# Kernel optimization log

Measured on AMD Instinct MI355X. Metric: run time of the kernel, lower is better.

Reference implementation:

```python
import jax, jax.numpy as jnp
import numpy as np

IN_DIM, HID, OUT, N_EXTRA, NTASKS, BATCH = 1024, 2048, 10, 3, 10, 4096
LOGSTD_MEAN, LOGSTD_STD = -6.0, 0.1


def setup_inputs() -> dict:
    key = jax.random.key(0)
    ks = jax.random.split(key, 20)
    n = lambda k, s: jax.random.normal(k, s, dtype=jnp.float32)
    return {
        "x": n(ks[0], (BATCH, IN_DIM)),
        # shared layer 0 (in_dim -> hidden)
        "mu_w0": n(ks[1], (HID, IN_DIM)) * (1.0 / np.sqrt(IN_DIM)),
        "ls_w0": LOGSTD_MEAN + LOGSTD_STD * n(ks[2], (HID, IN_DIM)),
        "mu_b0": n(ks[3], (HID,)) * 0.01,
        "ls_b0": LOGSTD_MEAN + LOGSTD_STD * n(ks[4], (HID,)),
        # shared layers 1..3 (hidden -> hidden), stacked
        "mu_w": n(ks[5], (N_EXTRA, HID, HID)) * (1.0 / np.sqrt(HID)),
        "ls_w": LOGSTD_MEAN + LOGSTD_STD * n(ks[6], (N_EXTRA, HID, HID)),
        "mu_b": n(ks[7], (N_EXTRA, HID)) * 0.01,
        "ls_b": LOGSTD_MEAN + LOGSTD_STD * n(ks[8], (N_EXTRA, HID)),
        # per-task heads (hidden -> out), stacked over tasks
        "mu_hw": n(ks[9], (NTASKS, OUT, HID)) * (1.0 / np.sqrt(HID)),
        "ls_hw": LOGSTD_MEAN + LOGSTD_STD * n(ks[10], (NTASKS, OUT, HID)),
        "mu_hb": n(ks[11], (NTASKS, OUT)) * 0.01,
        "ls_hb": LOGSTD_MEAN + LOGSTD_STD * n(ks[12], (NTASKS, OUT)),
        # reparameterization noise (one sample per forward, as in torch module)
        "eps_w0": n(ks[13], (HID, IN_DIM)),
        "eps_b0": n(ks[14], (HID,)),
        "eps_w": n(ks[15], (N_EXTRA, HID, HID)),
        "eps_b": n(ks[16], (N_EXTRA, HID)),
        "eps_hw": n(ks[17], (NTASKS, OUT, HID)),
        "eps_hb": n(ks[18], (NTASKS, OUT)),
        "task": jax.random.randint(ks[19], (BATCH,), 0, NTASKS, dtype=jnp.int64),
    }


def reference(x, mu_w0, ls_w0, mu_b0, ls_b0, mu_w, ls_w, mu_b, ls_b,
              mu_hw, ls_hw, mu_hb, ls_hb,
              eps_w0, eps_b0, eps_w, eps_b, eps_hw, eps_hb, task):
    # BayesianLinear: w = mu + exp(log_sigma) * eps
    w0 = mu_w0 + jnp.exp(ls_w0) * eps_w0          # [HID, IN]
    b0 = mu_b0 + jnp.exp(ls_b0) * eps_b0          # [HID]
    h = jax.nn.relu(x @ w0.T + b0)                # [B, HID]
    for i in range(N_EXTRA):                      # fixed small layer loop
        wi = mu_w[i] + jnp.exp(ls_w[i]) * eps_w[i]
        bi = mu_b[i] + jnp.exp(ls_b[i]) * eps_b[i]
        h = jax.nn.relu(h @ wi.T + bi)
    # multihead: compute every head, zero out non-matching rows (dense masked)
    hw = mu_hw + jnp.exp(ls_hw) * eps_hw          # [T, OUT, HID]
    hb = mu_hb + jnp.exp(ls_hb) * eps_hb          # [T, OUT]
    out_all = jnp.einsum('bh,toh->bto', h, hw) + hb[None]   # [B, T, OUT]
    onehot = (task[:, None] == jnp.arange(NTASKS)[None, :]).astype(h.dtype)
    return jnp.einsum('bto,bt->bo', out_all, onehot)        # [B, OUT]
```

## Files before the change

kernel.cpp:

```cpp
#include <hip/hip_runtime.h>
#include <cstdint>

#define BATCH 4096
#define IN_DIM 1024
#define HID 2048
#define OUT_DIM 10
#define NTASKS 10

typedef __bf16 bf16x8 __attribute__((ext_vector_type(8)));
typedef float f32x4 __attribute__((ext_vector_type(4)));
typedef __attribute__((address_space(3))) uint8_t lds_u8;
typedef const __attribute__((address_space(1))) uint8_t glb_u8;

__device__ __forceinline__ unsigned short f2bf(float f) {
    uint32_t u = __builtin_bit_cast(uint32_t, f);
    u += 0x7fffu + ((u >> 16) & 1u);
    return (unsigned short)(u >> 16);
}
__device__ __forceinline__ float bf2f(unsigned short h) {
    uint32_t u = ((uint32_t)h) << 16;
    return __builtin_bit_cast(float, u);
}


__global__ __launch_bounds__(256) void bl_transform(
    const float4* __restrict__ mu, const float4* __restrict__ ls,
    const float4* __restrict__ eps, ushort4* __restrict__ out)
{
    const int i0 = blockIdx.x * 1024 + threadIdx.x;
    const float4 m0 = mu[i0], m1 = mu[i0 + 256], m2 = mu[i0 + 512], m3 = mu[i0 + 768];
    const float4 l0 = ls[i0], l1 = ls[i0 + 256], l2 = ls[i0 + 512], l3 = ls[i0 + 768];
    const float4 e0 = eps[i0], e1 = eps[i0 + 256], e2 = eps[i0 + 512], e3 = eps[i0 + 768];
    ushort4 r0, r1, r2, r3;
    r0.x = f2bf(m0.x + __expf(l0.x) * e0.x); r0.y = f2bf(m0.y + __expf(l0.y) * e0.y);
    r0.z = f2bf(m0.z + __expf(l0.z) * e0.z); r0.w = f2bf(m0.w + __expf(l0.w) * e0.w);
    r1.x = f2bf(m1.x + __expf(l1.x) * e1.x); r1.y = f2bf(m1.y + __expf(l1.y) * e1.y);
    r1.z = f2bf(m1.z + __expf(l1.z) * e1.z); r1.w = f2bf(m1.w + __expf(l1.w) * e1.w);
    r2.x = f2bf(m2.x + __expf(l2.x) * e2.x); r2.y = f2bf(m2.y + __expf(l2.y) * e2.y);
    r2.z = f2bf(m2.z + __expf(l2.z) * e2.z); r2.w = f2bf(m2.w + __expf(l2.w) * e2.w);
    r3.x = f2bf(m3.x + __expf(l3.x) * e3.x); r3.y = f2bf(m3.y + __expf(l3.y) * e3.y);
    r3.z = f2bf(m3.z + __expf(l3.z) * e3.z); r3.w = f2bf(m3.w + __expf(l3.w) * e3.w);
    out[i0]       = r0;
    out[i0 + 256] = r1;
    out[i0 + 512] = r2;
    out[i0 + 768] = r3;
}

__global__ __launch_bounds__(256) void bl_cvt(
    const float4* __restrict__ in, ushort4* __restrict__ out)
{
    const int i0 = blockIdx.x * 1024 + threadIdx.x;
    const float4 v0 = in[i0], v1 = in[i0 + 256], v2 = in[i0 + 512], v3 = in[i0 + 768];
    ushort4 r0, r1, r2, r3;
    r0.x = f2bf(v0.x); r0.y = f2bf(v0.y); r0.z = f2bf(v0.z); r0.w = f2bf(v0.w);
    r1.x = f2bf(v1.x); r1.y = f2bf(v1.y); r1.z = f2bf(v1.z); r1.w = f2bf(v1.w);
    r2.x = f2bf(v2.x); r2.y = f2bf(v2.y); r2.z = f2bf(v2.z); r2.w = f2bf(v2.w);
    r3.x = f2bf(v3.x); r3.y = f2bf(v3.y); r3.z = f2bf(v3.z); r3.w = f2bf(v3.w);
    out[i0]       = r0;
    out[i0 + 256] = r1;
    out[i0 + 512] = r2;
    out[i0 + 768] = r3;
}

__global__ __launch_bounds__(256) void bl_small(
    const float* __restrict__ mu_b0, const float* __restrict__ ls_b0, const float* __restrict__ eps_b0,
    const float* __restrict__ mu_b,  const float* __restrict__ ls_b,  const float* __restrict__ eps_b,
    const float* __restrict__ mu_hw, const float* __restrict__ ls_hw, const float* __restrict__ eps_hw,
    const float* __restrict__ mu_hb, const float* __restrict__ ls_hb, const float* __restrict__ eps_hb,
    float* __restrict__ b_all, float* __restrict__ hw, float* __restrict__ hb)
{
    const int total = HID + 3*HID + NTASKS*OUT_DIM*HID + NTASKS*OUT_DIM;
    int i = blockIdx.x * blockDim.x + threadIdx.x;
    const int stride = gridDim.x * blockDim.x;
    for (; i < total; i += stride) {
        if (i < HID) {
            b_all[i] = mu_b0[i] + __expf(ls_b0[i]) * eps_b0[i];
        } else if (i < 4*HID) {
            const int j = i - HID;
            b_all[HID + j] = mu_b[j] + __expf(ls_b[j]) * eps_b[j];
        } else if (i < 4*HID + NTASKS*OUT_DIM*HID) {
            const int j = i - 4*HID;
            hw[j] = mu_hw[j] + __expf(ls_hw[j]) * eps_hw[j];
        } else {
            const int j = i - (4*HID + NTASKS*OUT_DIM*HID);
            hb[j] = mu_hb[j] + __expf(ls_hb[j]) * eps_hb[j];
        }
    }
}

#define BAR()        asm volatile("s_barrier" ::: "memory")
#define WAIT_LGKM0() do { asm volatile("s_waitcnt lgkmcnt(0)" ::: "memory"); __builtin_amdgcn_sched_barrier(0); } while (0)
#define RD_A(m, o)   (*(const bf16x8*)(ldsb + acur + (o) + (m)*2048))
#define RD_B(n, o)   (*(const bf16x8*)(ldsb + bcur + (o) + (n)*2048))
#define MFMA(d, va, vb) d = __builtin_amdgcn_mfma_f32_16x16x32_bf16(va, vb, d, 0, 0, 0)
#define STAGEI(i, kel, sl) \
    __builtin_amdgcn_global_load_lds((glb_u8*)(gsrc[i] + (kel)), \
        (lds_u8*)(ldsb + ldst[i] + (uint32_t)(sl) * smul[i]), 16, 0, 0)

__global__ __launch_bounds__(512, 2) void bl_gemm(
    const unsigned short* __restrict__ A,
    const unsigned short* __restrict__ B,
    const float* __restrict__ bias,
    unsigned short* __restrict__ C,
    int K)
{
    __shared__ unsigned short lds[49152];
    uint8_t* ldsb = (uint8_t*)lds;

    const int tid  = threadIdx.x;
    const int wave = tid >> 6;
    const int lane = tid & 63;
    const int swz = ((blockIdx.x & 7) << 5) | (blockIdx.x >> 3);
    const int bm = swz >> 4;
    const int bn = swz & 15;
    const int wr = wave >> 1;
    const int wc = wave & 1;

    const int lr8 = lane >> 3;
    const int ss  = (lane & 7) ^ lr8;
    const unsigned short* gsrc[6];
    uint32_t ldst[6], smul[6];
    #pragma unroll
    for (int i = 0; i < 6; ++i) {
        const int c = wave * 6 + i;
        if (c < 32) {
            gsrc[i] = A + (size_t)(bm * 256 + c * 8 + lr8) * K + ss * 8;
            ldst[i] = (uint32_t)c * 1024u;
            smul[i] = 32768u;
        } else {
            gsrc[i] = B + (size_t)(bn * 128 + (c - 32) * 8 + lr8) * K + ss * 8;
            ldst[i] = 65536u + (uint32_t)(c - 32) * 1024u;
            smul[i] = 16384u;
        }
    }

    const int rA = wr * 64 + (lane & 15);
    const int rB = wc * 64 + (lane & 15);
    const int ks = lane >> 4;
    const uint32_t aoff0 = (uint32_t)(rA * 128 + ((ks       ^ (rA & 7)) * 16));
    const uint32_t aoff1 = (uint32_t)(rA * 128 + (((4 | ks) ^ (rA & 7)) * 16));
    const uint32_t boff0 = (uint32_t)(rB * 128 + ((ks       ^ (rB & 7)) * 16));
    const uint32_t boff1 = (uint32_t)(rB * 128 + (((4 | ks) ^ (rB & 7)) * 16));

    f32x4 acc[4][4] = {};
    const int NT = K >> 6;

    STAGEI(0, 0, 0); STAGEI(1, 0, 0); STAGEI(2, 0, 0);
    STAGEI(3, 0, 0); STAGEI(4, 0, 0); STAGEI(5, 0, 0);
    __syncthreads();

    for (int t = 0; t < NT; ++t) {
        const int cur = t & 1, nxt = cur ^ 1;
        const uint32_t acur = (uint32_t)cur * 32768u;
        const uint32_t bcur = 65536u + (uint32_t)cur * 16384u;
        const bool pf = (t + 1 < NT);
        const int ktn = (t + 1) << 6;

        bf16x8 a0, a1, a2, a3, b0, b1, b2, b3;

        a0 = RD_A(0, aoff0); a1 = RD_A(1, aoff0);
        b0 = RD_B(0, boff0); b1 = RD_B(1, boff0); b2 = RD_B(2, boff0); b3 = RD_B(3, boff0);
        if (pf) { STAGEI(0, ktn, nxt); STAGEI(1, ktn, nxt); STAGEI(2, ktn, nxt); }
        BAR(); WAIT_LGKM0();
        __builtin_amdgcn_s_setprio(1);
        MFMA(acc[0][0], a0, b0); MFMA(acc[0][1], a0, b1); MFMA(acc[0][2], a0, b2); MFMA(acc[0][3], a0, b3);
        MFMA(acc[1][0], a1, b0); MFMA(acc[1][1], a1, b1); MFMA(acc[1][2], a1, b2); MFMA(acc[1][3], a1, b3);
        __builtin_amdgcn_s_setprio(0);
        BAR();

        a2 = RD_A(2, aoff0); a3 = RD_A(3, aoff0);
        if (pf) { STAGEI(3, ktn, nxt); STAGEI(4, ktn, nxt); STAGEI(5, ktn, nxt); }
        BAR(); WAIT_LGKM0();
        __builtin_amdgcn_s_setprio(1);
        MFMA(acc[2][0], a2, b0); MFMA(acc[2][1], a2, b1); MFMA(acc[2][2], a2, b2); MFMA(acc[2][3], a2, b3);
        MFMA(acc[3][0], a3, b0); MFMA(acc[3][1], a3, b1); MFMA(acc[3][2], a3, b2); MFMA(acc[3][3], a3, b3);
        __builtin_amdgcn_s_setprio(0);
        BAR();

        a0 = RD_A(0, aoff1); a1 = RD_A(1, aoff1);
        b0 = RD_B(0, boff1); b1 = RD_B(1, boff1); b2 = RD_B(2, boff1); b3 = RD_B(3, boff1);
        BAR(); WAIT_LGKM0();
        __builtin_amdgcn_s_setprio(1);
        MFMA(acc[0][0], a0, b0); MFMA(acc[0][1], a0, b1); MFMA(acc[0][2], a0, b2); MFMA(acc[0][3], a0, b3);
        MFMA(acc[1][0], a1, b0); MFMA(acc[1][1], a1, b1); MFMA(acc[1][2], a1, b2); MFMA(acc[1][3], a1, b3);
        __builtin_amdgcn_s_setprio(0);
        BAR();

        a2 = RD_A(2, aoff1); a3 = RD_A(3, aoff1);
        BAR(); WAIT_LGKM0();
        __builtin_amdgcn_s_setprio(1);
        MFMA(acc[2][0], a2, b0); MFMA(acc[2][1], a2, b1); MFMA(acc[2][2], a2, b2); MFMA(acc[2][3], a2, b3);
        MFMA(acc[3][0], a3, b0); MFMA(acc[3][1], a3, b1); MFMA(acc[3][2], a3, b2); MFMA(acc[3][3], a3, b3);
        __builtin_amdgcn_s_setprio(0);
        __syncthreads();
    }

    const int col0 = bn * 128 + wc * 64 + (lane & 15);
    const int row0 = bm * 256 + wr * 64 + ((lane >> 4) << 2);
    #pragma unroll
    for (int n = 0; n < 4; ++n) {
        const int col = col0 + n * 16;
        const float bv = bias[col];
        #pragma unroll
        for (int m = 0; m < 4; ++m) {
            #pragma unroll
            for (int j = 0; j < 4; ++j) {
                float v = acc[m][n][j] + bv;
                v = v > 0.0f ? v : 0.0f;
                C[(size_t)(row0 + m * 16 + j) * HID + col] = f2bf(v);
            }
        }
    }
}

__global__ __launch_bounds__(256) void bl_head(
    const unsigned short* __restrict__ h,
    const float* __restrict__ hw,
    const float* __restrict__ hb,
    const int* __restrict__ task,
    float* __restrict__ out)
{
    const int wave = threadIdx.x >> 6, lane = threadIdx.x & 63;
    const int b = blockIdx.x * 4 + wave;
    const int t = task[b];
    const float* w = hw + (size_t)t * OUT_DIM * HID;
    const unsigned short* hr = h + (size_t)b * HID;

    float acc[OUT_DIM];
    #pragma unroll
    for (int o = 0; o < OUT_DIM; ++o) acc[o] = 0.0f;

    #pragma unroll
    for (int i = 0; i < HID / 512; ++i) {
        const int k0 = (i * 64 + lane) * 8;
        const bf16x8 hv8 = *(const bf16x8*)(hr + k0);
        float hf[8];
        #pragma unroll
        for (int j = 0; j < 8; ++j) hf[j] = (float)hv8[j];
        #pragma unroll
        for (int o = 0; o < OUT_DIM; ++o) {
            const float4 w0 = *(const float4*)(w + (size_t)o * HID + k0);
            const float4 w1 = *(const float4*)(w + (size_t)o * HID + k0 + 4);
            acc[o] += hf[0]*w0.x + hf[1]*w0.y + hf[2]*w0.z + hf[3]*w0.w
                    + hf[4]*w1.x + hf[5]*w1.y + hf[6]*w1.z + hf[7]*w1.w;
        }
    }
    #pragma unroll
    for (int o = 0; o < OUT_DIM; ++o) {
        float v = acc[o];
        #pragma unroll
        for (int s = 32; s > 0; s >>= 1) v += __shfl_down(v, s, 64);
        if (lane == 0) out[(size_t)b * OUT_DIM + o] = v + hb[t * OUT_DIM + o];
    }
}


extern "C" void kernel_launch(void* const* d_in, const int* in_sizes, int n_in,
                              void* d_out, int out_size, void* d_ws, size_t ws_size,
                              hipStream_t stream)
{
    const float* x      = (const float*)d_in[0];
    const float* mu_w0  = (const float*)d_in[1];
    const float* ls_w0  = (const float*)d_in[2];
    const float* mu_b0  = (const float*)d_in[3];
    const float* ls_b0  = (const float*)d_in[4];
    const float* mu_w   = (const float*)d_in[5];
    const float* ls_w   = (const float*)d_in[6];
    const float* mu_b   = (const float*)d_in[7];
    const float* ls_b   = (const float*)d_in[8];
    const float* mu_hw  = (const float*)d_in[9];
    const float* ls_hw  = (const float*)d_in[10];
    const float* mu_hb  = (const float*)d_in[11];
    const float* ls_hb  = (const float*)d_in[12];
    const float* eps_w0 = (const float*)d_in[13];
    const float* eps_b0 = (const float*)d_in[14];
    const float* eps_w  = (const float*)d_in[15];
    const float* eps_b  = (const float*)d_in[16];
    const float* eps_hw = (const float*)d_in[17];
    const float* eps_hb = (const float*)d_in[18];
    const int*   task   = (const int*)d_in[19];

    uint8_t* ws = (uint8_t*)d_ws;
    constexpr size_t X_OFF  = 0;
    constexpr size_t W0_OFF = X_OFF  + (size_t)BATCH * IN_DIM * 2;
    constexpr size_t W_OFF  = W0_OFF + (size_t)HID * IN_DIM * 2;
    constexpr size_t H0_OFF = W_OFF  + (size_t)3 * HID * HID * 2;
    constexpr size_t H1_OFF = H0_OFF + (size_t)BATCH * HID * 2;
    constexpr size_t B_OFF  = H1_OFF + (size_t)BATCH * HID * 2;
    constexpr size_t HW_OFF = B_OFF  + (size_t)4 * HID * 4;
    constexpr size_t HB_OFF = HW_OFF + (size_t)NTASKS * OUT_DIM * HID * 4;

    unsigned short* xbf = (unsigned short*)(ws + X_OFF);
    unsigned short* w0b = (unsigned short*)(ws + W0_OFF);
    unsigned short* wb  = (unsigned short*)(ws + W_OFF);
    unsigned short* h0  = (unsigned short*)(ws + H0_OFF);
    unsigned short* h1  = (unsigned short*)(ws + H1_OFF);
    float* ball = (float*)(ws + B_OFF);
    float* hwf  = (float*)(ws + HW_OFF);
    float* hbf  = (float*)(ws + HB_OFF);

    bl_cvt<<<BATCH * IN_DIM / 4096, 256, 0, stream>>>((const float4*)x, (ushort4*)xbf);
    bl_transform<<<HID * IN_DIM / 4096, 256, 0, stream>>>(
        (const float4*)mu_w0, (const float4*)ls_w0, (const float4*)eps_w0, (ushort4*)w0b);
    bl_transform<<<3 * HID * HID / 4096, 256, 0, stream>>>(
        (const float4*)mu_w, (const float4*)ls_w, (const float4*)eps_w, (ushort4*)wb);
    bl_small<<<512, 256, 0, stream>>>(mu_b0, ls_b0, eps_b0, mu_b, ls_b, eps_b,
                                      mu_hw, ls_hw, eps_hw, mu_hb, ls_hb, eps_hb,
                                      ball, hwf, hbf);

    bl_gemm<<<256, 512, 0, stream>>>(xbf, w0b, ball,             h0, IN_DIM);
    bl_gemm<<<256, 512, 0, stream>>>(h0, wb,                     ball + HID,   h1, HID);
    bl_gemm<<<256, 512, 0, stream>>>(h1, wb + (size_t)HID*HID,   ball + 2*HID, h0, HID);
    bl_gemm<<<256, 512, 0, stream>>>(h0, wb + (size_t)2*HID*HID, ball + 3*HID, h1, HID);

    bl_head<<<BATCH / 4, 256, 0, stream>>>(h1, hwf, hbf, task, (float*)d_out);
}
```

Before: 214.0 us.

## Fuse preprocessing kernels into one persistent LDS-pipelined streaming kernel

Replaces the four preprocessing launches (x conversion, two weight reparameterisation transforms, and the small bias/head transform) with one kernel. It runs 1024 blocks whose waves each walk a contiguous range of float4 units spanning all segments. Each wave double-buffers the mu/logsigma/eps loads into LDS with global_load_lds and waits on the outstanding vector-memory count. The aim is to cut launch overhead and tail effects and to overlap loads with compute. In exchange it adds per-unit segment branching and LDS round-trips, and it switches the small-tensor path to float4 vector accesses.

```diff
diff --git a/kernel.cpp b/kernel.cpp
--- a/kernel.cpp
+++ b/kernel.cpp
@@ -17,75 +17,93 @@
     u += 0x7fffu + ((u >> 16) & 1u);
     return (unsigned short)(u >> 16);
 }
-__device__ __forceinline__ float bf2f(unsigned short h) {
-    uint32_t u = ((uint32_t)h) << 16;
-    return __builtin_bit_cast(float, u);
-}
-
-
-__global__ __launch_bounds__(256) void bl_transform(
-    const float4* __restrict__ mu, const float4* __restrict__ ls,
-    const float4* __restrict__ eps, ushort4* __restrict__ out)
+
+#define C1 1048576u
+#define C2 1572864u
+#define C3 4718592u
+#define C4 4769792u
+#define C5 4770304u
+#define GLL(src, ldsp) __builtin_amdgcn_global_load_lds((glb_u8*)(src), (lds_u8*)(ldsp), 16, 0, 0)
+
+__global__ __launch_bounds__(256) void bl_stream(
+    const float4* __restrict__ x4,
+    const float4* __restrict__ m0, const float4* __restrict__ l0, const float4* __restrict__ e0,
+    const float4* __restrict__ mw, const float4* __restrict__ lw, const float4* __restrict__ ew,
+    const float4* __restrict__ mh, const float4* __restrict__ lh, const float4* __restrict__ eh,
+    const float4* __restrict__ mb0, const float4* __restrict__ lb0, const float4* __restrict__ eb0,
+    const float4* __restrict__ mb, const float4* __restrict__ lb, const float4* __restrict__ eb,
+    const float* __restrict__ mu_hb, const float* __restrict__ ls_hb, const float* __restrict__ eps_hb,
+    ushort4* __restrict__ xbf4, ushort4* __restrict__ w0b4, ushort4* __restrict__ wb4,
+    float4* __restrict__ hw4, float4* __restrict__ b04, float4* __restrict__ bb4,
+    float* __restrict__ hbf)
 {
-    const int i0 = blockIdx.x * 1024 + threadIdx.x;
-    const float4 m0 = mu[i0], m1 = mu[i0 + 256], m2 = mu[i0 + 512], m3 = mu[i0 + 768];
-    const float4 l0 = ls[i0], l1 = ls[i0 + 256], l2 = ls[i0 + 512], l3 = ls[i0 + 768];
-    const float4 e0 = eps[i0], e1 = eps[i0 + 256], e2 = eps[i0 + 512], e3 = eps[i0 + 768];
-    ushort4 r0, r1, r2, r3;
-    r0.x = f2bf(m0.x + __expf(l0.x) * e0.x); r0.y = f2bf(m0.y + __expf(l0.y) * e0.y);
-    r0.z = f2bf(m0.z + __expf(l0.z) * e0.z); r0.w = f2bf(m0.w + __expf(l0.w) * e0.w);
-    r1.x = f2bf(m1.x + __expf(l1.x) * e1.x); r1.y = f2bf(m1.y + __expf(l1.y) * e1.y);
-    r1.z = f2bf(m1.z + __expf(l1.z) * e1.z); r1.w = f2bf(m1.w + __expf(l1.w) * e1.w);
-    r2.x = f2bf(m2.x + __expf(l2.x) * e2.x); r2.y = f2bf(m2.y + __expf(l2.y) * e2.y);
-    r2.z = f2bf(m2.z + __expf(l2.z) * e2.z); r2.w = f2bf(m2.w + __expf(l2.w) * e2.w);
-    r3.x = f2bf(m3.x + __expf(l3.x) * e3.x); r3.y = f2bf(m3.y + __expf(l3.y) * e3.y);
-    r3.z = f2bf(m3.z + __expf(l3.z) * e3.z); r3.w = f2bf(m3.w + __expf(l3.w) * e3.w);
-    out[i0]       = r0;
-    out[i0 + 256] = r1;
-    out[i0 + 512] = r2;
-    out[i0 + 768] = r3;
-}
-
-__global__ __launch_bounds__(256) void bl_cvt(
-    const float4* __restrict__ in, ushort4* __restrict__ out)
-{
-    const int i0 = blockIdx.x * 1024 + threadIdx.x;
-    const float4 v0 = in[i0], v1 = in[i0 + 256], v2 = in[i0 + 512], v3 = in[i0 + 768];
-    ushort4 r0, r1, r2, r3;
-    r0.x = f2bf(v0.x); r0.y = f2bf(v0.y); r0.z = f2bf(v0.z); r0.w = f2bf(v0.w);
-    r1.x = f2bf(v1.x); r1.y = f2bf(v1.y); r1.z = f2bf(v1.z); r1.w = f2bf(v1.w);
-    r2.x = f2bf(v2.x); r2.y = f2bf(v2.y); r2.z = f2bf(v2.z); r2.w = f2bf(v2.w);
-    r3.x = f2bf(v3.x); r3.y = f2bf(v3.y); r3.z = f2bf(v3.z); r3.w = f2bf(v3.w);
-    out[i0]       = r0;
-    out[i0 + 256] = r1;
-    out[i0 + 512] = r2;
-    out[i0 + 768] = r3;
-}
-
-__global__ __launch_bounds__(256) void bl_small(
-    const float* __restrict__ mu_b0, const float* __restrict__ ls_b0, const float* __restrict__ eps_b0,
-    const float* __restrict__ mu_b,  const float* __restrict__ ls_b,  const float* __restrict__ eps_b,
-    const float* __restrict__ mu_hw, const float* __restrict__ ls_hw, const float* __restrict__ eps_hw,
-    const float* __restrict__ mu_hb, const float* __restrict__ ls_hb, const float* __restrict__ eps_hb,
-    float* __restrict__ b_all, float* __restrict__ hw, float* __restrict__ hb)
-{
-    const int total = HID + 3*HID + NTASKS*OUT_DIM*HID + NTASKS*OUT_DIM;
-    int i = blockIdx.x * blockDim.x + threadIdx.x;
-    const int stride = gridDim.x * blockDim.x;
-    for (; i < total; i += stride) {
-        if (i < HID) {
-            b_all[i] = mu_b0[i] + __expf(ls_b0[i]) * eps_b0[i];
-        } else if (i < 4*HID) {
-            const int j = i - HID;
-            b_all[HID + j] = mu_b[j] + __expf(ls_b[j]) * eps_b[j];
-        } else if (i < 4*HID + NTASKS*OUT_DIM*HID) {
-            const int j = i - 4*HID;
-            hw[j] = mu_hw[j] + __expf(ls_hw[j]) * eps_hw[j];
+    __shared__ uint8_t sbuf[24576];
+    const int tid = threadIdx.x, wv = tid >> 6, ln = tid & 63;
+
+    if (blockIdx.x == 0 && tid < 100)
+        hbf[tid] = mu_hb[tid] + __expf(ls_hb[tid]) * eps_hb[tid];
+
+    const int w = blockIdx.x * 4 + wv;
+    const int niter = 18 + (w < 832 ? 1 : 0);
+    const uint32_t u0 = (uint32_t)(w * 18 + (w < 832 ? w : 832)) * 64u + (uint32_t)ln;
+    uint8_t* wl = sbuf + wv * 6144;
+
+    #define SEG_SRC(u, pa, pb, pc)                                               \
+        do {                                                                     \
+            uint32_t _u = (u);                                                   \
+            if (_u < C1)      { pa = x4 + _u; pb = pa; pc = pa; }                \
+            else if (_u < C2) { uint32_t v = _u - C1; pa = m0 + v; pb = l0 + v; pc = e0 + v; } \
+            else if (_u < C3) { uint32_t v = _u - C2; pa = mw + v; pb = lw + v; pc = ew + v; } \
+            else if (_u < C4) { uint32_t v = _u - C3; pa = mh + v; pb = lh + v; pc = eh + v; } \
+            else if (_u < C5) { uint32_t v = _u - C4; pa = mb0 + v; pb = lb0 + v; pc = eb0 + v; } \
+            else              { uint32_t v = _u - C5; pa = mb + v; pb = lb + v; pc = eb + v; } \
+        } while (0)
+
+    {
+        const float4 *pa, *pb, *pc;
+        SEG_SRC(u0, pa, pb, pc);
+        GLL(pa, wl); GLL(pb, wl + 1024); GLL(pc, wl + 2048);
+    }
+
+    for (int it = 0; it < niter; ++it) {
+        const int cb = it & 1;
+        if (it + 1 < niter) {
+            const float4 *pa, *pb, *pc;
+            SEG_SRC(u0 + (uint32_t)(it + 1) * 64u, pa, pb, pc);
+            uint8_t* nb = wl + (cb ^ 1) * 3072;
+            GLL(pa, nb); GLL(pb, nb + 1024); GLL(pc, nb + 2048);
+            asm volatile("s_waitcnt vmcnt(3)" ::: "memory");
         } else {
-            const int j = i - (4*HID + NTASKS*OUT_DIM*HID);
-            hb[j] = mu_hb[j] + __expf(ls_hb[j]) * eps_hb[j];
-        }
-    }
+            asm volatile("s_waitcnt vmcnt(0)" ::: "memory");
+        }
+        const uint8_t* rb = wl + cb * 3072;
+        const float4 m = *(const float4*)(rb + ln * 16);
+        const float4 l = *(const float4*)(rb + 1024 + ln * 16);
+        const float4 e = *(const float4*)(rb + 2048 + ln * 16);
+
+        const uint32_t u = u0 + (uint32_t)it * 64u;
+        if (u < C1) {
+            ushort4 r;
+            r.x = f2bf(m.x); r.y = f2bf(m.y); r.z = f2bf(m.z); r.w = f2bf(m.w);
+            xbf4[u] = r;
+        } else {
+            float4 t;
+            t.x = m.x + __expf(l.x) * e.x;
+            t.y = m.y + __expf(l.y) * e.y;
+            t.z = m.z + __expf(l.z) * e.z;
+            t.w = m.w + __expf(l.w) * e.w;
+            if (u < C3) {
+                ushort4 r;
+                r.x = f2bf(t.x); r.y = f2bf(t.y); r.z = f2bf(t.z); r.w = f2bf(t.w);
+                if (u < C2) w0b4[u - C1] = r; else wb4[u - C2] = r;
+            } else {
+                if (u < C4) hw4[u - C3] = t;
+                else if (u < C5) b04[u - C4] = t;
+                else bb4[u - C5] = t;
+            }
+        }
+    }
+    #undef SEG_SRC
 }
 
 #define BAR()        asm volatile("s_barrier" ::: "memory")
@@ -281,10 +299,11 @@
     const int*   task   = (const int*)d_in[19];
 
     uint8_t* ws = (uint8_t*)d_ws;
+    constexpr size_t HH     = (size_t)HID * HID;
     constexpr size_t X_OFF  = 0;
     constexpr size_t W0_OFF = X_OFF  + (size_t)BATCH * IN_DIM * 2;
     constexpr size_t W_OFF  = W0_OFF + (size_t)HID * IN_DIM * 2;
-    constexpr size_t H0_OFF = W_OFF  + (size_t)3 * HID * HID * 2;
+    constexpr size_t H0_OFF = W_OFF  + 3 * HH * 2;
     constexpr size_t H1_OFF = H0_OFF + (size_t)BATCH * HID * 2;
     constexpr size_t B_OFF  = H1_OFF + (size_t)BATCH * HID * 2;
     constexpr size_t HW_OFF = B_OFF  + (size_t)4 * HID * 4;
@@ -299,19 +318,21 @@
     float* hwf  = (float*)(ws + HW_OFF);
     float* hbf  = (float*)(ws + HB_OFF);
 
-    bl_cvt<<<BATCH * IN_DIM / 4096, 256, 0, stream>>>((const float4*)x, (ushort4*)xbf);
-    bl_transform<<<HID * IN_DIM / 4096, 256, 0, stream>>>(
-        (const float4*)mu_w0, (const float4*)ls_w0, (const float4*)eps_w0, (ushort4*)w0b);
-    bl_transform<<<3 * HID * HID / 4096, 256, 0, stream>>>(
-        (const float4*)mu_w, (const float4*)ls_w, (const float4*)eps_w, (ushort4*)wb);
-    bl_small<<<512, 256, 0, stream>>>(mu_b0, ls_b0, eps_b0, mu_b, ls_b, eps_b,
-                                      mu_hw, ls_hw, eps_hw, mu_hb, ls_hb, eps_hb,
-                                      ball, hwf, hbf);
+    bl_stream<<<1024, 256, 0, stream>>>(
+        (const float4*)x,
+        (const float4*)mu_w0, (const float4*)ls_w0, (const float4*)eps_w0,
+        (const float4*)mu_w,  (const float4*)ls_w,  (const float4*)eps_w,
+        (const float4*)mu_hw, (const float4*)ls_hw, (const float4*)eps_hw,
+        (const float4*)mu_b0, (const float4*)ls_b0, (const float4*)eps_b0,
+        (const float4*)mu_b,  (const float4*)ls_b,  (const float4*)eps_b,
+        mu_hb, ls_hb, eps_hb,
+        (ushort4*)xbf, (ushort4*)w0b, (ushort4*)wb,
+        (float4*)hwf, (float4*)ball, (float4*)(ball + HID), hbf);
 
     bl_gemm<<<256, 512, 0, stream>>>(xbf, w0b, ball,             h0, IN_DIM);
     bl_gemm<<<256, 512, 0, stream>>>(h0, wb,                     ball + HID,   h1, HID);
-    bl_gemm<<<256, 512, 0, stream>>>(h1, wb + (size_t)HID*HID,   ball + 2*HID, h0, HID);
-    bl_gemm<<<256, 512, 0, stream>>>(h0, wb + (size_t)2*HID*HID, ball + 3*HID, h1, HID);
+    bl_gemm<<<256, 512, 0, stream>>>(h1, wb + HH,                ball + 2*HID, h0, HID);
+    bl_gemm<<<256, 512, 0, stream>>>(h0, wb + 2*HH,              ball + 3*HID, h1, HID);
 
     bl_head<<<BATCH / 4, 256, 0, stream>>>(h1, hwf, hbf, task, (float*)d_out);
 }
```

Result: faster. 209.0 us (-2.3%).
